# Kernel tuning notes

Hardware: AMD Instinct MI355X
Metric: run time of the kernel (lower is better)

Reference implementation:

```python
import jax, jax.numpy as jnp
import numpy as np

B, S, V, H = 16, 256, 32, 256
LN_EPS = 1e-5


def setup_inputs() -> dict:
    key = jax.random.key(0)
    ks = jax.random.split(key, 8)
    sW = 1.0 / np.sqrt(H)
    return {
        "x": jax.random.normal(ks[0], (B, S, V, 1), jnp.float32),
        "W1": jax.random.normal(ks[1], (V, H), jnp.float32),          # linear1: input_size=1
        "b1": jax.random.normal(ks[2], (V, H), jnp.float32) * 0.1,
        "W2": jax.random.normal(ks[3], (V, H, H), jnp.float32) * sW,
        "b2": jax.random.normal(ks[4], (V, H), jnp.float32) * 0.1,
        "Wg": jax.random.normal(ks[5], (V, H, H), jnp.float32) * sW,
        "bg": jax.random.normal(ks[6], (V, H), jnp.float32) * 0.1,
        "gamma": jnp.ones((V, H), jnp.float32),
        "beta": jnp.zeros((V, H), jnp.float32),
        "Wa": jax.random.normal(ks[7], (H,), jnp.float32) * sW,
        "ba": jnp.zeros((1,), jnp.float32),
    }


def reference(x, W1, b1, W2, b2, Wg, bg, gamma, beta, Wa, ba):
    # Batched GRN over all variables at once (replaces the per-var Python loop).
    # x: [B,S,V,1]; linear1 with input_size=1 is a scalar-vector outer product.
    h = jax.nn.relu(x * W1 + b1)                                  # [B,S,V,H]
    h = jnp.einsum('bsvh,vhk->bsvk', h, W2) + b2                  # linear2
    gated = jax.nn.sigmoid(jnp.einsum('bsvh,vhk->bsvk', h, Wg) + bg) * h
    # residual is the raw scalar input (last dim 1), broadcast over H as in torch
    pre = x + gated                                               # [B,S,V,H]
    mu = jnp.mean(pre, axis=-1, keepdims=True)
    var = jnp.mean(jnp.square(pre - mu), axis=-1, keepdims=True)
    var_outputs = (pre - mu) * jax.lax.rsqrt(var + LN_EPS) * gamma + beta
    # softmax attention pooling over variables
    scores = jnp.einsum('bsvh,h->bsv', var_outputs, Wa) + ba[0]   # [B,S,V]
    attn = jax.nn.softmax(scores, axis=-1)[..., None]             # [B,S,V,1]
    vsn_out = jnp.sum(var_outputs * attn, axis=2)                 # [B,S,H]
    return vsn_out, attn
```

## Files before the change

### kernel.cpp

```cpp
#include <hip/hip_runtime.h>
#include <hip/hip_bf16.h>

typedef _Float16 f16;
typedef _Float16 f16x2 __attribute__((ext_vector_type(2)));
typedef _Float16 f16x4 __attribute__((ext_vector_type(4)));
typedef _Float16 f16x8 __attribute__((ext_vector_type(8)));
typedef float f32x4 __attribute__((ext_vector_type(4)));

#define T_TOK 4096
#define V_N 32
#define H_N 256
#define LN_EPS_F 1e-5f

__device__ __forceinline__ void gload16(const f16* g, f16* l) {
    __builtin_amdgcn_global_load_lds(
        (const __attribute__((address_space(1))) void*)g,
        (__attribute__((address_space(3))) void*)l, 16, 0, 0);
}
__device__ __forceinline__ void gload16f(const float* g, float* l) {
    __builtin_amdgcn_global_load_lds(
        (const __attribute__((address_space(1))) void*)g,
        (__attribute__((address_space(3))) void*)l, 16, 0, 0);
}

__global__ __launch_bounds__(256) void prep_transpose(
    const float* __restrict__ W2, const float* __restrict__ Wg,
    f16* __restrict__ W2t, f16* __restrict__ Wgt)
{
    __shared__ float tile[64][65];
    int bid = blockIdx.x;
    int w = bid >> 9;
    int rem = bid & 511;
    int v = rem >> 4;
    int kt = (rem >> 2) & 3;
    int nt = rem & 3;
    const float* src = w ? Wg : W2;
    f16* dst = w ? Wgt : W2t;
    const float* base = src + ((size_t)v * H_N + (size_t)kt * 64) * H_N + nt * 64;
    int tid = threadIdx.x;
    #pragma unroll
    for (int p = 0; p < 16; ++p) {
        int idx = p * 256 + tid;
        int r = idx >> 6, c = idx & 63;
        tile[r][c] = base[(size_t)r * H_N + c];
    }
    __syncthreads();
    f16* obase = dst + ((size_t)v * H_N + (size_t)nt * 64) * H_N + kt * 64;
    #pragma unroll
    for (int p = 0; p < 16; ++p) {
        int idx = p * 256 + tid;
        int r = idx >> 6, c = idx & 63;
        obase[(size_t)r * H_N + c] = (f16)tile[c][r];
    }
}

__global__ __launch_bounds__(256) void prep_w1(
    const float* __restrict__ W1, const float* __restrict__ b1,
    f16* __restrict__ W1h, f16* __restrict__ b1h)
{
    int i = blockIdx.x * 256 + threadIdx.x;
    W1h[i] = (f16)W1[i];
    b1h[i] = (f16)b1[i];
}

__global__ __launch_bounds__(512) void grn_h2(
    const float* __restrict__ x,
    const f16* __restrict__ W1h, const f16* __restrict__ b1h,
    const f16* __restrict__ W2t, const float* __restrict__ b2,
    f16* __restrict__ H2g)
{
    __shared__ f16 W2L[65536];
    __shared__ f16 W1L[256], b1L[256];
    __shared__ float b2L[256];

    int bid = blockIdx.x;
    int xcd = bid & 7, idx = bid >> 3;
    int v  = (xcd << 2) + (idx & 3);
    int t0 = (idx >> 2) * 512;
    int tid = threadIdx.x;
    int w = tid >> 6, lane = tid & 63;
    int lo = lane & 15, hi = lane >> 4;
    int q = w & 3, th = w >> 2;

    const f16* W2v = W2t + ((size_t)v << 16);

    int cs = (lane & 31) ^ ((w * 2 + (lane >> 5)) & 7);
    #pragma unroll
    for (int r = 0; r < 16; ++r)
        gload16(W2v + ((size_t)(r * 16 + w * 2 + (lane >> 5)) << 8) + (cs << 3),
                &W2L[(r * 16 + w * 2) << 8]);
    if (w == 0 && lane < 32) gload16(W1h + (v << 8) + (lane << 3), W1L);
    if (w == 1 && lane < 32) gload16(b1h + (v << 8) + (lane << 3), b1L);
    if (w == 2) gload16f(b2 + (v << 8) + (lane << 2), b2L);

    float xs[4][4];
    #pragma unroll
    for (int st = 0; st < 4; ++st)
        #pragma unroll
        for (int g = 0; g < 4; ++g)
            xs[st][g] = x[(size_t)(t0 + st * 128 + th * 64 + g * 16 + lo) * V_N + v];

    __syncthreads();

    #pragma unroll
    for (int st = 0; st < 4; ++st) {
        int m0 = t0 + st * 128 + th * 64;
        f16x8 x8[4];
        #pragma unroll
        for (int g = 0; g < 4; ++g) {
            f16 xh = (f16)xs[st][g];
            x8[g] = f16x8{ xh, xh, xh, xh, xh, xh, xh, xh };
        }
        f32x4 acc[4][4] = {};
        #pragma unroll
        for (int s = 0; s < 8; ++s) {
            f16x8 w8 = *(const f16x8*)&W1L[(s << 5) + (hi << 3)];
            f16x8 c8 = *(const f16x8*)&b1L[(s << 5) + (hi << 3)];
            f16x8 hv[4];
            #pragma unroll
            for (int g = 0; g < 4; ++g) {
                f16x8 t = x8[g] * w8 + c8;
                #pragma unroll
                for (int j = 0; j < 8; ++j) t[j] = t[j] > (f16)0 ? t[j] : (f16)0;
                hv[g] = t;
            }
            #pragma unroll
            for (int nf = 0; nf < 4; ++nf) {
                f16x8 af = *(const f16x8*)&W2L[((q * 64 + nf * 16 + lo) << 8)
                                               + ((((s << 2) + hi) ^ (lo & 7)) << 3)];
                #pragma unroll
                for (int g = 0; g < 4; ++g)
                    acc[g][nf] = __builtin_amdgcn_mfma_f32_16x16x32_f16(
                        af, hv[g], acc[g][nf], 0, 0, 0);
            }
        }
        #pragma unroll
        for (int nf = 0; nf < 4; ++nf) {
            int n0 = q * 64 + nf * 16 + (hi << 2);
            f32x4 b4 = *(const f32x4*)&b2L[n0];
            #pragma unroll
            for (int g = 0; g < 4; ++g) {
                f32x4 h = acc[g][nf] + b4;
                f16x4 hh = { (f16)h[0], (f16)h[1], (f16)h[2], (f16)h[3] };
                *(f16x4*)&H2g[((size_t)v * T_TOK + m0 + g * 16 + lo) * H_N + n0] = hh;
            }
        }
    }
}

__global__ __launch_bounds__(512, 2) void grn_out(
    const f16* __restrict__ Wgt, const float* __restrict__ bg,
    const float* __restrict__ gamma, const float* __restrict__ beta,
    const float* __restrict__ Wa, const float* __restrict__ ba,
    const f16* H2g,
    f16* VOg,
    float* __restrict__ scores)
{
    __shared__ __align__(16) f16 H2L[2][64 * 256];
    __shared__ float bgL[256], gmL[256], btL[256], waL[256];
    __shared__ float sqx[8][4][16][2];
    __shared__ float spxL[8][4][16];

    int bid = blockIdx.x;
    int xcd = bid & 7, idx = bid >> 3;
    int v  = (xcd << 2) + (idx & 3);
    int t0 = (idx >> 2) * 256;
    int tid = threadIdx.x;
    int w = tid >> 6, lane = tid & 63;
    int lo = lane & 15, hi = lane >> 4;

    const f16* Wgv = Wgt + ((size_t)v << 16);

    f16x8 afW[8][2];
    #pragma unroll
    for (int s = 0; s < 8; ++s)
        #pragma unroll
        for (int nf = 0; nf < 2; ++nf)
            afW[s][nf] = *(const f16x8*)&Wgv[((w * 32 + nf * 16 + lo) << 8)
                                             + (s << 5) + (hi << 3)];

    if (w == 0) gload16f(bg    + (v << 8) + (lane << 2), bgL);
    if (w == 1) gload16f(gamma + (v << 8) + (lane << 2), gmL);
    if (w == 2) gload16f(beta  + (v << 8) + (lane << 2), btL);
    if (w == 3) gload16f(Wa + (lane << 2), waL);
    float bav = ba[0];

    auto stage = [&](int tile, int buf) {
        #pragma unroll
        for (int i = 0; i < 4; ++i) {
            int r = w * 8 + i * 2 + (lane >> 5);
            int cg = (lane & 31) ^ (r & 31);
            gload16(H2g + ((size_t)v * T_TOK + t0 + tile * 64 + r) * H_N + (cg << 3),
                    &H2L[buf][(w * 8 + i * 2) << 8]);
        }
    };

    stage(0, 0);
    asm volatile("s_waitcnt vmcnt(0) lgkmcnt(0)" ::: "memory");
    __builtin_amdgcn_s_barrier();

    #pragma unroll
    for (int t = 0; t < 4; ++t) {
        const int buf = t & 1;
        if (t < 3) stage(t + 1, buf ^ 1);
        int m0 = t0 + t * 64;

        f32x4 acc[4][2] = {};
        #pragma unroll
        for (int s = 0; s < 8; ++s) {
            #pragma unroll
            for (int g = 0; g < 4; ++g) {
                int tok = g * 16 + lo;
                int slot = ((s << 2) + hi) ^ (tok & 31);
                f16x8 bf = *(const f16x8*)&H2L[buf][(tok << 8) + (slot << 3)];
                acc[g][0] = __builtin_amdgcn_mfma_f32_16x16x32_f16(
                    afW[s][0], bf, acc[g][0], 0, 0, 0);
                acc[g][1] = __builtin_amdgcn_mfma_f32_16x16x32_f16(
                    afW[s][1], bf, acc[g][1], 0, 0, 0);
            }
        }

        float sr[4] = {}, qr[4] = {};
        #pragma unroll
        for (int g = 0; g < 4; ++g) {
            int tok = g * 16 + lo;
            #pragma unroll
            for (int nf = 0; nf < 2; ++nf) {
                int n0 = w * 32 + nf * 16 + (hi << 2);
                f32x4 bgv = *(const f32x4*)&bgL[n0];
                int slot = ((w << 2) + (nf << 1) + (hi >> 1)) ^ (tok & 31);
                f16x4 h2v = *(const f16x4*)&H2L[buf][(tok << 8) + (slot << 3)
                                                     + ((hi & 1) << 2)];
                #pragma unroll
                for (int r = 0; r < 4; ++r) {
                    float a = acc[g][nf][r] + bgv[r];
                    float sg = 1.f / (1.f + __expf(-a));
                    float val = sg * (float)h2v[r];
                    acc[g][nf][r] = val;
                    sr[g] += val; qr[g] += val * val;
                }
            }
            sr[g] += __shfl_xor(sr[g], 16); sr[g] += __shfl_xor(sr[g], 32);
            qr[g] += __shfl_xor(qr[g], 16); qr[g] += __shfl_xor(qr[g], 32);
        }
        if (hi == 0) {
            #pragma unroll
            for (int g = 0; g < 4; ++g) {
                sqx[w][g][lo][0] = sr[g];
                sqx[w][g][lo][1] = qr[g];
            }
        }
        __syncthreads();

        float mu[4], inv[4];
        #pragma unroll
        for (int g = 0; g < 4; ++g) {
            float st = 0.f, qt = 0.f;
            #pragma unroll
            for (int ww = 0; ww < 8; ++ww) {
                st += sqx[ww][g][lo][0];
                qt += sqx[ww][g][lo][1];
            }
            mu[g] = st * (1.f / 256.f);
            float var = qt * (1.f / 256.f) - mu[g] * mu[g];
            inv[g] = rsqrtf(var + LN_EPS_F);
        }

        float sp[4] = {};
        #pragma unroll
        for (int g = 0; g < 4; ++g) {
            f16* VOr = VOg + ((size_t)v * T_TOK + m0 + g * 16 + lo) * H_N;
            #pragma unroll
            for (int nf = 0; nf < 2; ++nf) {
                int n0 = w * 32 + nf * 16 + (hi << 2);
                f32x4 gm = *(const f32x4*)&gmL[n0];
                f32x4 bt = *(const f32x4*)&btL[n0];
                f32x4 wa = *(const f32x4*)&waL[n0];
                f16x4 ov;
                #pragma unroll
                for (int r = 0; r < 4; ++r) {
                    float o = (acc[g][nf][r] - mu[g]) * inv[g] * gm[r] + bt[r];
                    sp[g] += o * wa[r];
                    ov[r] = (f16)o;
                }
                *(f16x4*)&VOr[n0] = ov;
            }
            sp[g] += __shfl_xor(sp[g], 16); sp[g] += __shfl_xor(sp[g], 32);
        }
        if (hi == 0) {
            #pragma unroll
            for (int g = 0; g < 4; ++g) spxL[w][g][lo] = sp[g];
        }
        asm volatile("s_waitcnt vmcnt(8) lgkmcnt(0)" ::: "memory");
        __builtin_amdgcn_s_barrier();

        if (w == 0 && hi == 0) {
            #pragma unroll
            for (int g = 0; g < 4; ++g) {
                float tsum = bav;
                #pragma unroll
                for (int ww = 0; ww < 8; ++ww) tsum += spxL[ww][g][lo];
                scores[(size_t)(m0 + g * 16 + lo) * V_N + v] = tsum;
            }
        }
    }
}

__global__ __launch_bounds__(128) void pool(
    const f16* __restrict__ VO,
    const float* __restrict__ scores,
    float* __restrict__ out)
{
    int t = blockIdx.x, tid = threadIdx.x;
    __shared__ float sc[V_N];
    if (tid < V_N) sc[tid] = scores[t * V_N + tid];
    __syncthreads();
    float mx = -1e30f;
    #pragma unroll
    for (int v = 0; v < V_N; ++v) mx = fmaxf(mx, sc[v]);
    float e[V_N];
    float sum = 0.f;
    #pragma unroll
    for (int v = 0; v < V_N; ++v) { e[v] = __expf(sc[v] - mx); sum += e[v]; }
    float isum = 1.f / sum;
    float a0 = 0.f, a1 = 0.f;
    #pragma unroll
    for (int v = 0; v < V_N; ++v) {
        f16x2 vv = *(const f16x2*)&VO[((size_t)v * T_TOK + t) * H_N + tid * 2];
        float ww = e[v] * isum;
        a0 = fmaf((float)vv[0], ww, a0);
        a1 = fmaf((float)vv[1], ww, a1);
    }
    *(float2*)&out[(size_t)t * H_N + tid * 2] = make_float2(a0, a1);
    if (tid < V_N)
        out[(size_t)T_TOK * H_N + (size_t)t * V_N + tid] = e[tid] * isum;
}

extern "C" void kernel_launch(void* const* d_in, const int* in_sizes, int n_in,
                              void* d_out, int out_size, void* d_ws, size_t ws_size,
                              hipStream_t stream)
{
    const float* x     = (const float*)d_in[0];
    const float* W1    = (const float*)d_in[1];
    const float* b1    = (const float*)d_in[2];
    const float* W2    = (const float*)d_in[3];
    const float* b2    = (const float*)d_in[4];
    const float* Wg    = (const float*)d_in[5];
    const float* bg    = (const float*)d_in[6];
    const float* gamma = (const float*)d_in[7];
    const float* beta  = (const float*)d_in[8];
    const float* Wa    = (const float*)d_in[9];
    const float* ba    = (const float*)d_in[10];
    float* out = (float*)d_out;

    char* ws = (char*)d_ws;
    f16* W2t = (f16*)ws;
    f16* Wgt = (f16*)(ws + ((size_t)4 << 20));
    f16* H2g = (f16*)(ws + ((size_t)8 << 20));
    float* scores = (float*)(ws + ((size_t)72 << 20));
    f16* W1h = (f16*)(ws + ((size_t)72 << 20) + (512 << 10));
    f16* b1h = (f16*)(ws + ((size_t)72 << 20) + (528 << 10));
    const size_t NEED = ((size_t)137 << 20);
    f16* VOg = (ws_size >= NEED) ? (f16*)(ws + ((size_t)73 << 20)) : H2g;

    prep_transpose<<<1024, 256, 0, stream>>>(W2, Wg, W2t, Wgt);
    prep_w1<<<32, 256, 0, stream>>>(W1, b1, W1h, b1h);
    grn_h2<<<256, 512, 0, stream>>>(x, W1h, b1h, W2t, b2, H2g);
    grn_out<<<512, 512, 0, stream>>>(Wgt, bg, gamma, beta, Wa, ba, H2g, VOg, scores);
    pool<<<4096, 128, 0, stream>>>(VOg, scores, out);
}
```

Baseline: 119.7 us.

## Shrink per-block token tiles and raise grid size for both GRN kernels

grn_h2 no longer stages the full 128KB W2 slice in LDS. Each wave now holds its W2 fragments in registers and handles one 64-token tile, launched over 2048 blocks. grn_out drops its double-buffered four-tile loop in favour of one 64-token tile per block over 2048 blocks, with launch bounds raised to 4 blocks per CU. The aim is higher occupancy and more parallelism, at the cost of reloading weights from global/L2 much more often and losing the intra-block load/compute overlap.

Result: slower. 141.4 us (+18.1%).

```diff
diff --git a/kernel.cpp b/kernel.cpp
--- a/kernel.cpp
+++ b/kernel.cpp
@@ -63,92 +63,67 @@
     b1h[i] = (f16)b1[i];
 }
 
-__global__ __launch_bounds__(512) void grn_h2(
+__global__ __launch_bounds__(512, 4) void grn_h2(
     const float* __restrict__ x,
     const f16* __restrict__ W1h, const f16* __restrict__ b1h,
     const f16* __restrict__ W2t, const float* __restrict__ b2,
     f16* __restrict__ H2g)
 {
-    __shared__ f16 W2L[65536];
-    __shared__ f16 W1L[256], b1L[256];
-    __shared__ float b2L[256];
-
     int bid = blockIdx.x;
     int xcd = bid & 7, idx = bid >> 3;
     int v  = (xcd << 2) + (idx & 3);
-    int t0 = (idx >> 2) * 512;
+    int m0 = (idx >> 2) * 64;
     int tid = threadIdx.x;
     int w = tid >> 6, lane = tid & 63;
     int lo = lane & 15, hi = lane >> 4;
-    int q = w & 3, th = w >> 2;
 
     const f16* W2v = W2t + ((size_t)v << 16);
 
-    int cs = (lane & 31) ^ ((w * 2 + (lane >> 5)) & 7);
-    #pragma unroll
-    for (int r = 0; r < 16; ++r)
-        gload16(W2v + ((size_t)(r * 16 + w * 2 + (lane >> 5)) << 8) + (cs << 3),
-                &W2L[(r * 16 + w * 2) << 8]);
-    if (w == 0 && lane < 32) gload16(W1h + (v << 8) + (lane << 3), W1L);
-    if (w == 1 && lane < 32) gload16(b1h + (v << 8) + (lane << 3), b1L);
-    if (w == 2) gload16f(b2 + (v << 8) + (lane << 2), b2L);
-
-    float xs[4][4];
-    #pragma unroll
-    for (int st = 0; st < 4; ++st)
-        #pragma unroll
-        for (int g = 0; g < 4; ++g)
-            xs[st][g] = x[(size_t)(t0 + st * 128 + th * 64 + g * 16 + lo) * V_N + v];
-
-    __syncthreads();
-
-    #pragma unroll
-    for (int st = 0; st < 4; ++st) {
-        int m0 = t0 + st * 128 + th * 64;
-        f16x8 x8[4];
-        #pragma unroll
-        for (int g = 0; g < 4; ++g) {
-            f16 xh = (f16)xs[st][g];
-            x8[g] = f16x8{ xh, xh, xh, xh, xh, xh, xh, xh };
-        }
-        f32x4 acc[4][4] = {};
-        #pragma unroll
-        for (int s = 0; s < 8; ++s) {
-            f16x8 w8 = *(const f16x8*)&W1L[(s << 5) + (hi << 3)];
-            f16x8 c8 = *(const f16x8*)&b1L[(s << 5) + (hi << 3)];
-            f16x8 hv[4];
+    f16x8 afW[8][2];
+    #pragma unroll
+    for (int s = 0; s < 8; ++s)
+        #pragma unroll
+        for (int nf = 0; nf < 2; ++nf)
+            afW[s][nf] = *(const f16x8*)&W2v[((w * 32 + nf * 16 + lo) << 8)
+                                             + (s << 5) + (hi << 3)];
+
+    f16 xh[4];
+    #pragma unroll
+    for (int g = 0; g < 4; ++g)
+        xh[g] = (f16)x[(size_t)(m0 + g * 16 + lo) * V_N + v];
+
+    f32x4 acc[4][2] = {};
+    #pragma unroll
+    for (int s = 0; s < 8; ++s) {
+        f16x8 w8 = *(const f16x8*)&W1h[(v << 8) + (s << 5) + (hi << 3)];
+        f16x8 c8 = *(const f16x8*)&b1h[(v << 8) + (s << 5) + (hi << 3)];
+        #pragma unroll
+        for (int g = 0; g < 4; ++g) {
+            f16x8 t;
             #pragma unroll
-            for (int g = 0; g < 4; ++g) {
-                f16x8 t = x8[g] * w8 + c8;
-                #pragma unroll
-                for (int j = 0; j < 8; ++j) t[j] = t[j] > (f16)0 ? t[j] : (f16)0;
-                hv[g] = t;
+            for (int j = 0; j < 8; ++j) {
+                f16 h = xh[g] * w8[j] + c8[j];
+                t[j] = h > (f16)0 ? h : (f16)0;
             }
-            #pragma unroll
-            for (int nf = 0; nf < 4; ++nf) {
-                f16x8 af = *(const f16x8*)&W2L[((q * 64 + nf * 16 + lo) << 8)
-                                               + ((((s << 2) + hi) ^ (lo & 7)) << 3)];
-                #pragma unroll
-                for (int g = 0; g < 4; ++g)
-                    acc[g][nf] = __builtin_amdgcn_mfma_f32_16x16x32_f16(
-                        af, hv[g], acc[g][nf], 0, 0, 0);
-            }
-        }
-        #pragma unroll
-        for (int nf = 0; nf < 4; ++nf) {
-            int n0 = q * 64 + nf * 16 + (hi << 2);
-            f32x4 b4 = *(const f32x4*)&b2L[n0];
-            #pragma unroll
-            for (int g = 0; g < 4; ++g) {
-                f32x4 h = acc[g][nf] + b4;
-                f16x4 hh = { (f16)h[0], (f16)h[1], (f16)h[2], (f16)h[3] };
-                *(f16x4*)&H2g[((size_t)v * T_TOK + m0 + g * 16 + lo) * H_N + n0] = hh;
-            }
-        }
-    }
-}
-
-__global__ __launch_bounds__(512, 2) void grn_out(
+            acc[g][0] = __builtin_amdgcn_mfma_f32_16x16x32_f16(afW[s][0], t, acc[g][0], 0, 0, 0);
+            acc[g][1] = __builtin_amdgcn_mfma_f32_16x16x32_f16(afW[s][1], t, acc[g][1], 0, 0, 0);
+        }
+    }
+
+    #pragma unroll
+    for (int nf = 0; nf < 2; ++nf) {
+        int n0 = w * 32 + nf * 16 + (hi << 2);
+        f32x4 b4 = *(const f32x4*)&b2[(v << 8) + n0];
+        #pragma unroll
+        for (int g = 0; g < 4; ++g) {
+            f32x4 h = acc[g][nf] + b4;
+            f16x4 hh = { (f16)h[0], (f16)h[1], (f16)h[2], (f16)h[3] };
+            *(f16x4*)&H2g[((size_t)v * T_TOK + m0 + g * 16 + lo) * H_N + n0] = hh;
+        }
+    }
+}
+
+__global__ __launch_bounds__(512, 4) void grn_out(
     const f16* __restrict__ Wgt, const float* __restrict__ bg,
     const float* __restrict__ gamma, const float* __restrict__ beta,
     const float* __restrict__ Wa, const float* __restrict__ ba,
@@ -156,7 +131,7 @@
     f16* VOg,
     float* __restrict__ scores)
 {
-    __shared__ __align__(16) f16 H2L[2][64 * 256];
+    __shared__ __align__(16) f16 H2L[64 * 256];
     __shared__ float bgL[256], gmL[256], btL[256], waL[256];
     __shared__ float sqx[8][4][16][2];
     __shared__ float spxL[8][4][16];
@@ -164,7 +139,7 @@
     int bid = blockIdx.x;
     int xcd = bid & 7, idx = bid >> 3;
     int v  = (xcd << 2) + (idx & 3);
-    int t0 = (idx >> 2) * 256;
+    int m0 = (idx >> 2) * 64;
     int tid = threadIdx.x;
     int w = tid >> 6, lane = tid & 63;
     int lo = lane & 15, hi = lane >> 4;
@@ -179,129 +154,111 @@
             afW[s][nf] = *(const f16x8*)&Wgv[((w * 32 + nf * 16 + lo) << 8)
                                              + (s << 5) + (hi << 3)];
 
+    #pragma unroll
+    for (int i = 0; i < 4; ++i) {
+        int r = w * 8 + i * 2 + (lane >> 5);
+        int cg = (lane & 31) ^ (r & 31);
+        gload16(H2g + ((size_t)v * T_TOK + m0 + r) * H_N + (cg << 3),
+                &H2L[(w * 8 + i * 2) << 8]);
+    }
     if (w == 0) gload16f(bg    + (v << 8) + (lane << 2), bgL);
     if (w == 1) gload16f(gamma + (v << 8) + (lane << 2), gmL);
     if (w == 2) gload16f(beta  + (v << 8) + (lane << 2), btL);
     if (w == 3) gload16f(Wa + (lane << 2), waL);
     float bav = ba[0];
-
-    auto stage = [&](int tile, int buf) {
-        #pragma unroll
-        for (int i = 0; i < 4; ++i) {
-            int r = w * 8 + i * 2 + (lane >> 5);
-            int cg = (lane & 31) ^ (r & 31);
-            gload16(H2g + ((size_t)v * T_TOK + t0 + tile * 64 + r) * H_N + (cg << 3),
-                    &H2L[buf][(w * 8 + i * 2) << 8]);
-        }
-    };
-
-    stage(0, 0);
-    asm volatile("s_waitcnt vmcnt(0) lgkmcnt(0)" ::: "memory");
-    __builtin_amdgcn_s_barrier();
-
-    #pragma unroll
-    for (int t = 0; t < 4; ++t) {
-        const int buf = t & 1;
-        if (t < 3) stage(t + 1, buf ^ 1);
-        int m0 = t0 + t * 64;
-
-        f32x4 acc[4][2] = {};
-        #pragma unroll
-        for (int s = 0; s < 8; ++s) {
+    __syncthreads();
+
+    f32x4 acc[4][2] = {};
+    #pragma unroll
+    for (int s = 0; s < 8; ++s) {
+        #pragma unroll
+        for (int g = 0; g < 4; ++g) {
+            int tok = g * 16 + lo;
+            int slot = ((s << 2) + hi) ^ (tok & 31);
+            f16x8 bf = *(const f16x8*)&H2L[(tok << 8) + (slot << 3)];
+            acc[g][0] = __builtin_amdgcn_mfma_f32_16x16x32_f16(afW[s][0], bf, acc[g][0], 0, 0, 0);
+            acc[g][1] = __builtin_amdgcn_mfma_f32_16x16x32_f16(afW[s][1], bf, acc[g][1], 0, 0, 0);
+        }
+    }
+
+    float sr[4] = {}, qr[4] = {};
+    #pragma unroll
+    for (int g = 0; g < 4; ++g) {
+        int tok = g * 16 + lo;
+        #pragma unroll
+        for (int nf = 0; nf < 2; ++nf) {
+            int n0 = w * 32 + nf * 16 + (hi << 2);
+            f32x4 bgv = *(const f32x4*)&bgL[n0];
+            int slot = ((w << 2) + (nf << 1) + (hi >> 1)) ^ (tok & 31);
+            f16x4 h2v = *(const f16x4*)&H2L[(tok << 8) + (slot << 3) + ((hi & 1) << 2)];
             #pragma unroll
-            for (int g = 0; g < 4; ++g) {
-                int tok = g * 16 + lo;
-                int slot = ((s << 2) + hi) ^ (tok & 31);
-                f16x8 bf = *(const f16x8*)&H2L[buf][(tok << 8) + (slot << 3)];
-                acc[g][0] = __builtin_amdgcn_mfma_f32_16x16x32_f16(
-                    afW[s][0], bf, acc[g][0], 0, 0, 0);
-                acc[g][1] = __builtin_amdgcn_mfma_f32_16x16x32_f16(
-                    afW[s][1], bf, acc[g][1], 0, 0, 0);
+            for (int r = 0; r < 4; ++r) {
+                float a = acc[g][nf][r] + bgv[r];
+                float sg = 1.f / (1.f + __expf(-a));
+                float val = sg * (float)h2v[r];
+                acc[g][nf][r] = val;
+                sr[g] += val; qr[g] += val * val;
             }
         }
-
-        float sr[4] = {}, qr[4] = {};
-        #pragma unroll
-        for (int g = 0; g < 4; ++g) {
-            int tok = g * 16 + lo;
+        sr[g] += __shfl_xor(sr[g], 16); sr[g] += __shfl_xor(sr[g], 32);
+        qr[g] += __shfl_xor(qr[g], 16); qr[g] += __shfl_xor(qr[g], 32);
+    }
+    if (hi == 0) {
+        #pragma unroll
+        for (int g = 0; g < 4; ++g) {
+            sqx[w][g][lo][0] = sr[g];
+            sqx[w][g][lo][1] = qr[g];
+        }
+    }
+    __syncthreads();
+
+    float mu[4], inv[4];
+    #pragma unroll
+    for (int g = 0; g < 4; ++g) {
+        float st = 0.f, qt = 0.f;
+        #pragma unroll
+        for (int ww = 0; ww < 8; ++ww) {
+            st += sqx[ww][g][lo][0];
+            qt += sqx[ww][g][lo][1];
+        }
+        mu[g] = st * (1.f / 256.f);
+        float var = qt * (1.f / 256.f) - mu[g] * mu[g];
+        inv[g] = rsqrtf(var + LN_EPS_F);
+    }
+
+    float sp[4] = {};
+    #pragma unroll
+    for (int g = 0; g < 4; ++g) {
+        f16* VOr = VOg + ((size_t)v * T_TOK + m0 + g * 16 + lo) * H_N;
+        #pragma unroll
+        for (int nf = 0; nf < 2; ++nf) {
+            int n0 = w * 32 + nf * 16 + (hi << 2);
+            f32x4 gm = *(const f32x4*)&gmL[n0];
+            f32x4 bt = *(const f32x4*)&btL[n0];
+            f32x4 wa = *(const f32x4*)&waL[n0];
+            f16x4 ov;
             #pragma unroll
-            for (int nf = 0; nf < 2; ++nf) {
-                int n0 = w * 32 + nf * 16 + (hi << 2);
-                f32x4 bgv = *(const f32x4*)&bgL[n0];
-                int slot = ((w << 2) + (nf << 1) + (hi >> 1)) ^ (tok & 31);
-                f16x4 h2v = *(const f16x4*)&H2L[buf][(tok << 8) + (slot << 3)
-                                                     + ((hi & 1) << 2)];
-                #pragma unroll
-                for (int r = 0; r < 4; ++r) {
-                    float a = acc[g][nf][r] + bgv[r];
-                    float sg = 1.f / (1.f + __expf(-a));
-                    float val = sg * (float)h2v[r];
-                    acc[g][nf][r] = val;
-                    sr[g] += val; qr[g] += val * val;
-                }
+            for (int r = 0; r < 4; ++r) {
+                float o = (acc[g][nf][r] - mu[g]) * inv[g] * gm[r] + bt[r];
+                sp[g] += o * wa[r];
+                ov[r] = (f16)o;
             }
-            sr[g] += __shfl_xor(sr[g], 16); sr[g] += __shfl_xor(sr[g], 32);
-            qr[g] += __shfl_xor(qr[g], 16); qr[g] += __shfl_xor(qr[g], 32);
-        }
-        if (hi == 0) {
+            *(f16x4*)&VOr[n0] = ov;
+        }
+        sp[g] += __shfl_xor(sp[g], 16); sp[g] += __shfl_xor(sp[g], 32);
+    }
+    if (hi == 0) {
+        #pragma unroll
+        for (int g = 0; g < 4; ++g) spxL[w][g][lo] = sp[g];
+    }
+    __syncthreads();
+    if (w == 0 && hi == 0) {
+        #pragma unroll
+        for (int g = 0; g < 4; ++g) {
+            float tsum = bav;
             #pragma unroll
-            for (int g = 0; g < 4; ++g) {
-                sqx[w][g][lo][0] = sr[g];
-                sqx[w][g][lo][1] = qr[g];
-            }
-        }
-        __syncthreads();
-
-        float mu[4], inv[4];
-        #pragma unroll
-        for (int g = 0; g < 4; ++g) {
-            float st = 0.f, qt = 0.f;
-            #pragma unroll
-            for (int ww = 0; ww < 8; ++ww) {
-                st += sqx[ww][g][lo][0];
-                qt += sqx[ww][g][lo][1];
-            }
-            mu[g] = st * (1.f / 256.f);
-            float var = qt * (1.f / 256.f) - mu[g] * mu[g];
-            inv[g] = rsqrtf(var + LN_EPS_F);
-        }
-
-        float sp[4] = {};
-        #pragma unroll
-        for (int g = 0; g < 4; ++g) {
-            f16* VOr = VOg + ((size_t)v * T_TOK + m0 + g * 16 + lo) * H_N;
-            #pragma unroll
-            for (int nf = 0; nf < 2; ++nf) {
-                int n0 = w * 32 + nf * 16 + (hi << 2);
-                f32x4 gm = *(const f32x4*)&gmL[n0];
-                f32x4 bt = *(const f32x4*)&btL[n0];
-                f32x4 wa = *(const f32x4*)&waL[n0];
-                f16x4 ov;
-                #pragma unroll
-                for (int r = 0; r < 4; ++r) {
-                    float o = (acc[g][nf][r] - mu[g]) * inv[g] * gm[r] + bt[r];
-                    sp[g] += o * wa[r];
-                    ov[r] = (f16)o;
-                }
-                *(f16x4*)&VOr[n0] = ov;
-            }
-            sp[g] += __shfl_xor(sp[g], 16); sp[g] += __shfl_xor(sp[g], 32);
-        }
-        if (hi == 0) {
-            #pragma unroll
-            for (int g = 0; g < 4; ++g) spxL[w][g][lo] = sp[g];
-        }
-        asm volatile("s_waitcnt vmcnt(8) lgkmcnt(0)" ::: "memory");
-        __builtin_amdgcn_s_barrier();
-
-        if (w == 0 && hi == 0) {
-            #pragma unroll
-            for (int g = 0; g < 4; ++g) {
-                float tsum = bav;
-                #pragma unroll
-                for (int ww = 0; ww < 8; ++ww) tsum += spxL[ww][g][lo];
-                scores[(size_t)(m0 + g * 16 + lo) * V_N + v] = tsum;
-            }
+            for (int ww = 0; ww < 8; ++ww) tsum += spxL[ww][g][lo];
+            scores[(size_t)(m0 + g * 16 + lo) * V_N + v] = tsum;
         }
     }
 }
@@ -365,7 +322,7 @@
 
     prep_transpose<<<1024, 256, 0, stream>>>(W2, Wg, W2t, Wgt);
     prep_w1<<<32, 256, 0, stream>>>(W1, b1, W1h, b1h);
-    grn_h2<<<256, 512, 0, stream>>>(x, W1h, b1h, W2t, b2, H2g);
-    grn_out<<<512, 512, 0, stream>>>(Wgt, bg, gamma, beta, Wa, ba, H2g, VOg, scores);
+    grn_h2<<<2048, 512, 0, stream>>>(x, W1h, b1h, W2t, b2, H2g);
+    grn_out<<<2048, 512, 0, stream>>>(Wgt, bg, gamma, beta, Wa, ba, H2g, VOg, scores);
     pool<<<4096, 128, 0, stream>>>(VOg, scores, out);
 }
```
